# Kernel tuning notes

Hardware: AMD Instinct MI355X
Metric: run time of the kernel (lower is better)

Reference implementation:

```python
import jax, jax.numpy as jnp
import numpy as np

B, T, C, H = 4, 2048, 1024, 16
D = C // H

def setup_inputs() -> dict:
    key = jax.random.key(0)
    k1, k2, k3, k4 = jax.random.split(key, 4)
    s = 1.0 / np.sqrt(C)
    return {
        "x": jax.random.normal(k1, (B, T, C), dtype=jnp.float32),
        "W_qkv": jax.random.normal(k2, (3 * C, C), dtype=jnp.float32) * s,
        "W_out": jax.random.normal(k3, (C, C), dtype=jnp.float32) * s,
        "b_out": jax.random.normal(k4, (C,), dtype=jnp.float32) * s,
    }

def reference(x, W_qkv, W_out, b_out):
    Bx, Tx, Cx = x.shape
    # qkv projection (torch Linear: y = x @ W.T), bias=False
    qkv = x @ W_qkv.T                               # [B,T,3C]
    q, k, v = jnp.split(qkv, 3, axis=-1)
    def heads(t):
        return t.reshape(Bx, Tx, H, D).transpose(0, 2, 1, 3)  # [B,H,T,D]
    q, k, v = heads(q), heads(k), heads(v)
    scale = 1.0 / jnp.sqrt(jnp.asarray(D, dtype=x.dtype))
    scores = jnp.einsum("bhqd,bhkd->bhqk", q, k) * scale      # [B,H,T,T]
    causal = jnp.tril(jnp.ones((Tx, Tx), dtype=bool))
    scores = jnp.where(causal[None, None], scores, -jnp.inf)
    attn = jax.nn.softmax(scores, axis=-1)                    # dropout p=0 (eval)
    out = jnp.einsum("bhqk,bhkd->bhqd", attn, v)              # [B,H,T,D]
    out = out.transpose(0, 2, 1, 3).reshape(Bx, Tx, Cx)       # [B,T,C]
    return out @ W_out.T + b_out
```

## Files before the change

kernel.cpp:

```cpp
#include <hip/hip_runtime.h>


typedef __attribute__((ext_vector_type(8))) __bf16 bf16x8;
typedef __attribute__((ext_vector_type(4))) float f32x4;
typedef __attribute__((ext_vector_type(16))) float f32x16;

__device__ __forceinline__ unsigned short f2bf(float f) {
  union { float f; unsigned u; } v; v.f = f;
  unsigned r = v.u + 0x7fffu + ((v.u >> 16) & 1u);
  return (unsigned short)(r >> 16);
}

__device__ __forceinline__ unsigned cvtpk(float lo, float hi) {
  unsigned r;
  asm("v_cvt_pk_bf16_f32 %0, %1, %2" : "=v"(r) : "v"(lo), "v"(hi));
  return r;
}

__device__ __forceinline__ float fexp2(float x) {
  float r;
  asm("v_exp_f32 %0, %1" : "=v"(r) : "v"(x));
  return r;
}
__device__ __forceinline__ float max3f(float a, float b, float c) {
  return fmaxf(fmaxf(a, b), c);
}

__device__ __forceinline__ void gld16(const void* g, void* l) {
  __builtin_amdgcn_global_load_lds(
      (const __attribute__((address_space(1))) void*)g,
      (__attribute__((address_space(3))) void*)l, 16, 0, 0);
}

__device__ __forceinline__ f32x4 mfma16(bf16x8 a, bf16x8 b, f32x4 c) {
  return __builtin_amdgcn_mfma_f32_16x16x32_bf16(a, b, c, 0, 0, 0);
}
__device__ __forceinline__ f32x16 mfma32(bf16x8 a, bf16x8 b, f32x16 c) {
  return __builtin_amdgcn_mfma_f32_32x32x16_bf16(a, b, c, 0, 0, 0);
}

__global__ __launch_bounds__(256) void cast_f32_bf16(
    const float* __restrict__ src, unsigned short* __restrict__ dst, int n) {
  int i = (blockIdx.x * 256 + threadIdx.x) * 4;
  if (i >= n) return;
  float4 v = *(const float4*)(src + i);
  ushort4 o;
  o.x = f2bf(v.x); o.y = f2bf(v.y); o.z = f2bf(v.z); o.w = f2bf(v.w);
  *(ushort4*)(dst + i) = o;
}

__device__ __forceinline__ bf16x8 ldsw128(const char* mat, int row, int cb) {
  return *(const bf16x8*)(mat + row * 128 + (cb ^ ((row & 7) << 4)));
}

#define PH_SYNC_A() do { __builtin_amdgcn_s_barrier();              \
    asm volatile("s_waitcnt lgkmcnt(0)" ::: "memory");              \
    __builtin_amdgcn_sched_barrier(0); } while (0)
#define PH_SYNC_B() do { __builtin_amdgcn_s_barrier();              \
    __builtin_amdgcn_sched_barrier(0); } while (0)
#define VMC6() asm volatile("s_waitcnt vmcnt(6)" ::: "memory")
#define VMC0() asm volatile("s_waitcnt vmcnt(0)" ::: "memory")

#define QUAD(MH, NH, AF, BF) do {                                   \
    __builtin_amdgcn_s_setprio(1);                                  \
    _Pragma("unroll") for (int mt = 0; mt < 4; ++mt)                \
    _Pragma("unroll") for (int nt = 0; nt < 2; ++nt)                \
    _Pragma("unroll") for (int kk = 0; kk < 2; ++kk)                \
      acc[(MH)*4+mt][(NH)*2+nt] =                                   \
          mfma16(AF[mt][kk], BF[nt][kk], acc[(MH)*4+mt][(NH)*2+nt]);\
    __builtin_amdgcn_s_setprio(0);                                  \
  } while (0)

__device__ __forceinline__ void stage_half(const char* gbase, char* mat,
                                           int kt, int half, int tid) {
#pragma unroll
  for (int q = 0; q < 2; ++q) {
    const int r = half * 128 + q * 64 + (tid >> 3);
    const int cb = (tid & 7) * 16;
    gld16(gbase + (size_t)r * 2048 + kt * 128 + (cb ^ ((r & 7) << 4)),
          mat + r * 128 + cb);
  }
}

__device__ __forceinline__ void rdA(bf16x8 aF[4][2], const char* mat,
                                    int wm, int mh, int lr, int lg) {
#pragma unroll
  for (int mt = 0; mt < 4; ++mt) {
    const int row = mh * 128 + wm * 64 + mt * 16 + lr;
#pragma unroll
    for (int kk = 0; kk < 2; ++kk)
      aF[mt][kk] = ldsw128(mat, row, kk * 64 + lg * 16);
  }
}
__device__ __forceinline__ void rdB(bf16x8 bF[2][2], const char* mat,
                                    int wn, int nh, int lr, int lg) {
#pragma unroll
  for (int nt = 0; nt < 2; ++nt) {
    const int row = wn * 64 + nh * 32 + nt * 16 + lr;
#pragma unroll
    for (int kk = 0; kk < 2; ++kk)
      bF[nt][kk] = ldsw128(mat, row, kk * 64 + lg * 16);
  }
}

template <int MODE>
__global__ __launch_bounds__(512, 2) void gemm8p(
    const unsigned short* __restrict__ A, const unsigned short* __restrict__ Bm,
    unsigned short* __restrict__ qo, unsigned short* __restrict__ ko,
    unsigned short* __restrict__ vo,
    const float* __restrict__ bias, float* __restrict__ fout) {
  __shared__ char lds[131072];
  const int tid = threadIdx.x;
  const int w = tid >> 6, l = tid & 63, lr = l & 15, lg = l >> 4;
  const int wm = w >> 2, wn = w & 3;
  constexpr int GX = (MODE == 0) ? 12 : 4;
  constexpr int NWG = GX * 32;
  const int L = blockIdx.x + blockIdx.y * GX;
  const int logical = (L & 7) * (NWG >> 3) + (L >> 3);
  const int m0 = (logical / GX) * 256, n0 = (logical % GX) * 256;
  const char* Ag = (const char*)A + (size_t)m0 * 2048;
  const char* Bg = (const char*)Bm + (size_t)n0 * 2048;
  char* A0 = lds;           char* B0 = lds + 32768;
  char* A1 = lds + 65536;   char* B1 = lds + 98304;

  f32x4 acc[8][4];
  f32x4 zero = {0.f, 0.f, 0.f, 0.f};
#pragma unroll
  for (int i = 0; i < 8; i++)
#pragma unroll
    for (int jj = 0; jj < 4; jj++) acc[i][jj] = zero;

  stage_half(Ag, A0, 0, 0, tid);
  stage_half(Ag, A0, 0, 1, tid);
  stage_half(Bg, B0, 0, 0, tid);
  stage_half(Bg, B0, 0, 1, tid);
  stage_half(Ag, A1, 1, 0, tid);
  stage_half(Bg, B1, 1, 0, tid);
  stage_half(Bg, B1, 1, 1, tid);
  VMC6();
  __builtin_amdgcn_s_barrier();
  __builtin_amdgcn_sched_barrier(0);

  for (int j = 0; j < 8; ++j) {
    const int t0 = 2 * j, t1 = 2 * j + 1;
    const bool more = (j < 7);
    bf16x8 aF[4][2], b0F[2][2], b1F[2][2];

    rdA(aF, A0, wm, 0, lr, lg);
    rdB(b0F, B0, wn, 0, lr, lg);
    stage_half(Ag, A1, t1, 1, tid);
    PH_SYNC_A();
    QUAD(0, 0, aF, b0F);
    PH_SYNC_B();
    rdB(b1F, B0, wn, 1, lr, lg);
    if (more) stage_half(Ag, A0, t0 + 2, 0, tid);
    PH_SYNC_A();
    QUAD(0, 1, aF, b1F);
    PH_SYNC_B();
    rdA(aF, A0, wm, 1, lr, lg);
    if (more) stage_half(Bg, B0, t0 + 2, 0, tid);
    PH_SYNC_A();
    QUAD(1, 1, aF, b1F);
    PH_SYNC_B();
    if (more) stage_half(Bg, B0, t0 + 2, 1, tid);
    PH_SYNC_A();
    QUAD(1, 0, aF, b0F);
    if (more) VMC6(); else VMC0();
    PH_SYNC_B();
    rdA(aF, A1, wm, 0, lr, lg);
    rdB(b0F, B1, wn, 0, lr, lg);
    if (more) stage_half(Ag, A0, t0 + 2, 1, tid);
    PH_SYNC_A();
    QUAD(0, 0, aF, b0F);
    PH_SYNC_B();
    rdB(b1F, B1, wn, 1, lr, lg);
    if (more) stage_half(Ag, A1, t1 + 2, 0, tid);
    PH_SYNC_A();
    QUAD(0, 1, aF, b1F);
    PH_SYNC_B();
    rdA(aF, A1, wm, 1, lr, lg);
    if (more) stage_half(Bg, B1, t1 + 2, 0, tid);
    PH_SYNC_A();
    QUAD(1, 1, aF, b1F);
    PH_SYNC_B();
    if (more) stage_half(Bg, B1, t1 + 2, 1, tid);
    PH_SYNC_A();
    QUAD(1, 0, aF, b0F);
    if (more) VMC6();
    PH_SYNC_B();
  }

#pragma unroll
  for (int mt8 = 0; mt8 < 8; ++mt8) {
    const int mh = mt8 >> 2, mt = mt8 & 3;
#pragma unroll
    for (int nt4 = 0; nt4 < 4; ++nt4) {
      int n = n0 + wn * 64 + nt4 * 16 + lr;
      int mbase = m0 + mh * 128 + wm * 64 + mt * 16 + lg * 4;
      if (MODE == 0) {
        int ty = n >> 10, cc = n & 1023;
        int h = cc >> 6, dd = cc & 63;
        unsigned short* dst = (ty == 0) ? qo : ((ty == 1) ? ko : vo);
        float sc = (ty == 0) ? 0.18033688011111687f : 1.0f;
#pragma unroll
        for (int i = 0; i < 4; i++) {
          int m = mbase + i;
          int b = m >> 11, tt = m & 2047;
          dst[(((size_t)(b * 16 + h)) * 2048 + tt) * 64 + dd] =
              f2bf(acc[mt8][nt4][i] * sc);
        }
      } else {
        float bv = bias[n];
#pragma unroll
        for (int i = 0; i < 4; i++) {
          int m = mbase + i;
          fout[(size_t)m * 1024 + n] = acc[mt8][nt4][i] + bv;
        }
      }
    }
  }
}

__global__ __launch_bounds__(256) void transpose_v64(
    const unsigned short* __restrict__ v, unsigned short* __restrict__ vt) {
  __shared__ unsigned short tile[64 * 72];
  int bh = blockIdx.y, t0 = blockIdx.x * 64;
  const unsigned short* vp = v + (size_t)bh * 2048 * 64;
  unsigned short* vtp = vt + (size_t)bh * 64 * 2048;
  int tid = threadIdx.x;
#pragma unroll
  for (int it = 0; it < 2; ++it) {
    int s = tid + it * 256;
    int r = s >> 3, c = (s & 7) * 8;
    *(uint4*)(tile + r * 72 + c) = *(const uint4*)(vp + (size_t)(t0 + r) * 64 + c);
  }
  __syncthreads();
#pragma unroll
  for (int it = 0; it < 2; ++it) {
    int s = tid + it * 256;
    int d = s >> 3, c = (s & 7) * 8;
    unsigned short tmp[8];
#pragma unroll
    for (int j = 0; j < 8; j++) tmp[j] = tile[(c + j) * 72 + d];
    *(uint4*)(vtp + (size_t)d * 2048 + t0 + c) = *(uint4*)tmp;
  }
}

__device__ __forceinline__ bf16x8 ldsw(const char* base, int row, int cb) {
  return *(const bf16x8*)(base + row * 128 + (cb ^ ((row & 7) << 4)));
}

__global__ __launch_bounds__(512, 4) void attn_causal(
    const unsigned short* __restrict__ qg, const unsigned short* __restrict__ kg,
    const unsigned short* __restrict__ vtg, unsigned short* __restrict__ og) {
  __shared__ char lds[32768];
  const int tid = threadIdx.x;
  const int w = tid >> 6, l = tid & 63, lo = l & 31, hi = l >> 5;
  const int bh = blockIdx.x;
  const int qc = (0x31204657u >> (blockIdx.y * 4)) & 7;
  const int q0 = qc * 256;
  const int nkv = qc * 4 + 4;
  const int b = bh >> 4, h = bh & 15;
  const char* kpB = (const char*)(kg + (size_t)bh * 131072);
  const char* vpB = (const char*)(vtg + (size_t)bh * 131072);
  const unsigned short* qp = qg + (size_t)bh * 131072;
  const int qrow = q0 + 8 * lo + w;

  bf16x8 qf[4];
#pragma unroll
  for (int c = 0; c < 4; ++c)
    qf[c] = *(const bf16x8*)(qp + (size_t)qrow * 64 + hi * 8 + c * 16);

  f32x16 ov[2];
#pragma unroll
  for (int r = 0; r < 16; ++r) { ov[0][r] = 0.f; ov[1][r] = 0.f; }
  const f32x16 zz = {0.f, 0.f, 0.f, 0.f, 0.f, 0.f, 0.f, 0.f,
                     0.f, 0.f, 0.f, 0.f, 0.f, 0.f, 0.f, 0.f};
  float m = -__builtin_inff(), lsum = 0.f;

  const int srow = tid >> 3;
  const int scb = ((tid & 7) * 16) ^ ((srow & 7) << 4);

  gld16(kpB + (size_t)srow * 128 + scb, lds + tid * 16);
  gld16(vpB + (size_t)srow * 4096 + scb, lds + 8192 + tid * 16);
  __syncthreads();

  for (int kt = 0; kt < nkv; ++kt) {
    const int k0 = kt * 64;
    if (kt + 1 < nkv) {
      char* nb = lds + ((kt + 1) & 1) * 16384;
      gld16(kpB + (size_t)(k0 + 64 + srow) * 128 + scb, nb + tid * 16);
      gld16(vpB + (size_t)srow * 4096 + (size_t)(k0 + 64) * 2 + scb, nb + 8192 + tid * 16);
    }
    const char* Kbuf = lds + (kt & 1) * 16384;
    const char* Vbuf = Kbuf + 8192;

    f32x16 sv[2];
    __builtin_amdgcn_s_setprio(1);
#pragma unroll
    for (int c = 0; c < 4; ++c) {
      bf16x8 kf0 = ldsw(Kbuf, lo, hi * 16 + c * 32);
      bf16x8 kf1 = ldsw(Kbuf, 32 + lo, hi * 16 + c * 32);
      if (c == 0) {
        sv[0] = mfma32(kf0, qf[0], zz);
        sv[1] = mfma32(kf1, qf[0], zz);
      } else {
        sv[0] = mfma32(kf0, qf[c], sv[0]);
        sv[1] = mfma32(kf1, qf[c], sv[1]);
      }
    }
    __builtin_amdgcn_s_setprio(0);

    if (kt >= nkv - 4) {
#pragma unroll
      for (int t = 0; t < 2; ++t)
#pragma unroll
        for (int r = 0; r < 16; ++r) {
          int kgl = k0 + t * 32 + (r & 3) + 8 * (r >> 2) + 4 * hi;
          if (kgl > qrow) sv[t][r] = -__builtin_inff();
        }
    }

    float t0m = max3f(sv[0][0], sv[0][1], sv[0][2]);
    float t1m = max3f(sv[0][3], sv[0][4], sv[0][5]);
    float t2m = max3f(sv[0][6], sv[0][7], sv[0][8]);
    float t3m = max3f(sv[0][9], sv[0][10], sv[0][11]);
    float t4m = max3f(sv[0][12], sv[0][13], sv[0][14]);
    float t5m = max3f(sv[0][15], sv[1][0], sv[1][1]);
    float t6m = max3f(sv[1][2], sv[1][3], sv[1][4]);
    float t7m = max3f(sv[1][5], sv[1][6], sv[1][7]);
    float t8m = max3f(sv[1][8], sv[1][9], sv[1][10]);
    float t9m = max3f(sv[1][11], sv[1][12], sv[1][13]);
    float tam = fmaxf(sv[1][14], sv[1][15]);
    float u0 = max3f(t0m, t1m, t2m);
    float u1 = max3f(t3m, t4m, t5m);
    float u2 = max3f(t6m, t7m, t8m);
    float u3 = fmaxf(t9m, tam);
    float tm = fmaxf(max3f(u0, u1, u2), u3);
    tm = fmaxf(tm, __shfl_xor(tm, 32, 64));

    if (!__all(tm <= m + 8.f)) {
      float nm = fmaxf(fmaxf(m, tm), -1e30f);
      float f = fexp2(m - nm);
      m = nm;
      lsum *= f;
#pragma unroll
      for (int r = 0; r < 16; ++r) { ov[0][r] *= f; ov[1][r] *= f; }
    }

    float ps0 = 0.f, ps1 = 0.f, ps2 = 0.f, ps3 = 0.f;
#pragma unroll
    for (int t = 0; t < 2; ++t)
#pragma unroll
      for (int r = 0; r < 16; r += 4) {
        float p0 = fexp2(sv[t][r + 0] - m);
        float p1 = fexp2(sv[t][r + 1] - m);
        float p2 = fexp2(sv[t][r + 2] - m);
        float p3 = fexp2(sv[t][r + 3] - m);
        sv[t][r + 0] = p0; sv[t][r + 1] = p1;
        sv[t][r + 2] = p2; sv[t][r + 3] = p3;
        ps0 += p0; ps1 += p1; ps2 += p2; ps3 += p3;
      }
    lsum += (ps0 + ps1) + (ps2 + ps3);

    __builtin_amdgcn_s_setprio(1);
#pragma unroll
    for (int c = 0; c < 4; ++c) {
      const int t = c >> 1, rb = (c & 1) * 8;
      unsigned wA = cvtpk(sv[t][rb + 0], sv[t][rb + 1]);
      unsigned wB = cvtpk(sv[t][rb + 2], sv[t][rb + 3]);
      unsigned wC = cvtpk(sv[t][rb + 4], sv[t][rb + 5]);
      unsigned wD = cvtpk(sv[t][rb + 6], sv[t][rb + 7]);
      asm volatile("v_permlane32_swap_b32 %0, %1" : "+v"(wA), "+v"(wC));
      asm volatile("v_permlane32_swap_b32 %0, %1" : "+v"(wB), "+v"(wD));
      union { uint4 u; bf16x8 h; } pc;
      pc.u.x = wA; pc.u.y = wB; pc.u.z = wC; pc.u.w = wD;
      bf16x8 vf0 = ldsw(Vbuf, lo, hi * 16 + c * 32);
      bf16x8 vf1 = ldsw(Vbuf, 32 + lo, hi * 16 + c * 32);
      ov[0] = mfma32(vf0, pc.h, ov[0]);
      ov[1] = mfma32(vf1, pc.h, ov[1]);
    }
    __builtin_amdgcn_s_setprio(0);
    __syncthreads();
  }

  float lt = lsum + __shfl_xor(lsum, 32, 64);
  float inv = 1.0f / lt;
  char* outl = lds + w * 4096;
#pragma unroll
  for (int t2 = 0; t2 < 2; ++t2)
#pragma unroll
    for (int rp = 0; rp < 8; ++rp) {
      const int r = rp * 2;
      const int d0 = (r & 3) + 8 * (r >> 2) + 4 * hi + 32 * t2;
      unsigned pw = cvtpk(ov[t2][r] * inv, ov[t2][r + 1] * inv);
      *(unsigned*)(outl + lo * 128 + ((d0 * 2) ^ ((lo & 7) << 4))) = pw;
    }
  __syncthreads();
  {
    const int qi = l >> 1, cbb = (l & 1) * 64;
    const int t = q0 + 8 * qi + w;
    unsigned short* gp = og + ((size_t)(b * 2048 + t)) * 1024 + h * 64 + (cbb >> 1);
#pragma unroll
    for (int i = 0; i < 4; ++i) {
      uint4 vdat = *(const uint4*)(outl + qi * 128 + ((cbb + i * 16) ^ ((qi & 7) << 4)));
      *(uint4*)(gp + i * 8) = vdat;
    }
  }
}

extern "C" void kernel_launch(void* const* d_in, const int* in_sizes, int n_in,
                              void* d_out, int out_size, void* d_ws, size_t ws_size,
                              hipStream_t stream) {
  const float* x = (const float*)d_in[0];
  const float* Wqkv = (const float*)d_in[1];
  const float* Wout = (const float*)d_in[2];
  const float* bout = (const float*)d_in[3];
  float* out = (float*)d_out;
  char* ws = (char*)d_ws;

  unsigned short* xb = (unsigned short*)(ws);
  unsigned short* wqb = (unsigned short*)(ws + 16777216);
  unsigned short* wob = (unsigned short*)(ws + 23068672);
  unsigned short* qb = (unsigned short*)(ws + 25165824);
  unsigned short* kb = (unsigned short*)(ws + 41943040);
  unsigned short* vb = (unsigned short*)(ws + 58720256);
  unsigned short* vtb = xb;
  unsigned short* ogb = vb;

  cast_f32_bf16<<<8192, 256, 0, stream>>>(x, xb, 8388608);
  cast_f32_bf16<<<3072, 256, 0, stream>>>(Wqkv, wqb, 3145728);
  cast_f32_bf16<<<1024, 256, 0, stream>>>(Wout, wob, 1048576);

  gemm8p<0><<<dim3(12, 32), 512, 0, stream>>>(xb, wqb, qb, kb, vb, nullptr, nullptr);
  transpose_v64<<<dim3(32, 64), 256, 0, stream>>>(vb, vtb);
  attn_causal<<<dim3(64, 8), 512, 0, stream>>>(qb, kb, vtb, ogb);
  gemm8p<1><<<dim3(4, 32), 512, 0, stream>>>(ogb, wob, nullptr, nullptr, nullptr, bout, out);
}
```

Before: 169.0 us.

## Fuse V transpose into QKV GEMM epilogue with LDS-staged coalesced stores

The QKV GEMM epilogue now stages its bf16 output tile in LDS with an XOR swizzle. It then writes Q/K rows as coalesced 16-byte chunks, and writes V already transposed into the [B,H,D,T] layout that attention reads. This drops the separate transpose kernel and its extra global round trip, and replaces the scattered 2-byte global stores. The workgroup-to-tile mapping also changes so each XCD group covers contiguous M tiles. The cost is an extra barrier and LDS traffic in the epilogue, and the workspace buffers are remapped.

```diff
diff --git a/kernel.cpp b/kernel.cpp
--- a/kernel.cpp
+++ b/kernel.cpp
@@ -51,6 +51,9 @@
 
 __device__ __forceinline__ bf16x8 ldsw128(const char* mat, int row, int cb) {
   return *(const bf16x8*)(mat + row * 128 + (cb ^ ((row & 7) << 4)));
+}
+__device__ __forceinline__ int swz512(int r) {
+  return ((r & 7) << 4) ^ (((r >> 3) & 3) << 7);
 }
 
 #define PH_SYNC_A() do { __builtin_amdgcn_s_barrier();              \
@@ -114,10 +117,10 @@
   const int w = tid >> 6, l = tid & 63, lr = l & 15, lg = l >> 4;
   const int wm = w >> 2, wn = w & 3;
   constexpr int GX = (MODE == 0) ? 12 : 4;
-  constexpr int NWG = GX * 32;
   const int L = blockIdx.x + blockIdx.y * GX;
-  const int logical = (L & 7) * (NWG >> 3) + (L >> 3);
-  const int m0 = (logical / GX) * 256, n0 = (logical % GX) * 256;
+  const int x = L & 7, i8 = L >> 3;
+  const int m0 = (x * 4 + (i8 & 3)) * 256;
+  const int n0 = (i8 >> 2) * 256;
   const char* Ag = (const char*)A + (size_t)m0 * 2048;
   const char* Bg = (const char*)Bm + (size_t)n0 * 2048;
   char* A0 = lds;           char* B0 = lds + 32768;
@@ -190,59 +193,85 @@
     PH_SYNC_B();
   }
 
-#pragma unroll
-  for (int mt8 = 0; mt8 < 8; ++mt8) {
-    const int mh = mt8 >> 2, mt = mt8 & 3;
-#pragma unroll
-    for (int nt4 = 0; nt4 < 4; ++nt4) {
-      int n = n0 + wn * 64 + nt4 * 16 + lr;
-      int mbase = m0 + mh * 128 + wm * 64 + mt * 16 + lg * 4;
-      if (MODE == 0) {
-        int ty = n >> 10, cc = n & 1023;
-        int h = cc >> 6, dd = cc & 63;
-        unsigned short* dst = (ty == 0) ? qo : ((ty == 1) ? ko : vo);
-        float sc = (ty == 0) ? 0.18033688011111687f : 1.0f;
-#pragma unroll
-        for (int i = 0; i < 4; i++) {
-          int m = mbase + i;
-          int b = m >> 11, tt = m & 2047;
-          dst[(((size_t)(b * 16 + h)) * 2048 + tt) * 64 + dd] =
+  if (MODE == 1) {
+#pragma unroll
+    for (int mt8 = 0; mt8 < 8; ++mt8) {
+      const int mh = mt8 >> 2, mt = mt8 & 3;
+#pragma unroll
+      for (int nt4 = 0; nt4 < 4; ++nt4) {
+        int n = n0 + wn * 64 + nt4 * 16 + lr;
+        int mbase = m0 + mh * 128 + wm * 64 + mt * 16 + lg * 4;
+        float bv = bias[n];
+#pragma unroll
+        for (int i = 0; i < 4; i++)
+          fout[(size_t)(mbase + i) * 1024 + n] = acc[mt8][nt4][i] + bv;
+      }
+    }
+    return;
+  }
+
+  const int ty = n0 >> 10;
+  const int hbase = (n0 & 1023) >> 6;
+  const int bb = m0 >> 11;
+  const int tloc = m0 & 2047;
+  const float sc = (ty == 0) ? 0.18033688011111687f : 1.0f;
+
+  if (ty < 2) {
+#pragma unroll
+    for (int mt8 = 0; mt8 < 8; ++mt8) {
+      const int mh = mt8 >> 2, mt = mt8 & 3;
+#pragma unroll
+      for (int nt4 = 0; nt4 < 4; ++nt4) {
+        const int col = wn * 64 + nt4 * 16 + lr;
+#pragma unroll
+        for (int i = 0; i < 4; ++i) {
+          const int row = mh * 128 + wm * 64 + mt * 16 + lg * 4 + i;
+          *(unsigned short*)(lds + row * 512 + ((col * 2) ^ swz512(row))) =
               f2bf(acc[mt8][nt4][i] * sc);
         }
-      } else {
-        float bv = bias[n];
-#pragma unroll
-        for (int i = 0; i < 4; i++) {
-          int m = mbase + i;
-          fout[(size_t)m * 1024 + n] = acc[mt8][nt4][i] + bv;
-        }
-      }
-    }
-  }
-}
-
-__global__ __launch_bounds__(256) void transpose_v64(
-    const unsigned short* __restrict__ v, unsigned short* __restrict__ vt) {
-  __shared__ unsigned short tile[64 * 72];
-  int bh = blockIdx.y, t0 = blockIdx.x * 64;
-  const unsigned short* vp = v + (size_t)bh * 2048 * 64;
-  unsigned short* vtp = vt + (size_t)bh * 64 * 2048;
-  int tid = threadIdx.x;
-#pragma unroll
-  for (int it = 0; it < 2; ++it) {
-    int s = tid + it * 256;
-    int r = s >> 3, c = (s & 7) * 8;
-    *(uint4*)(tile + r * 72 + c) = *(const uint4*)(vp + (size_t)(t0 + r) * 64 + c);
-  }
-  __syncthreads();
-#pragma unroll
-  for (int it = 0; it < 2; ++it) {
-    int s = tid + it * 256;
-    int d = s >> 3, c = (s & 7) * 8;
-    unsigned short tmp[8];
-#pragma unroll
-    for (int j = 0; j < 8; j++) tmp[j] = tile[(c + j) * 72 + d];
-    *(uint4*)(vtp + (size_t)d * 2048 + t0 + c) = *(uint4*)tmp;
+      }
+    }
+    __builtin_amdgcn_s_barrier();
+    unsigned short* dst = (ty == 0) ? qo : ko;
+    const int hi = tid >> 7, r = tid & 127;
+    unsigned short* gp =
+        dst + (((size_t)(bb * 16 + hbase + hi)) * 2048 + tloc + 2 * r) * 64;
+#pragma unroll
+    for (int rr = 0; rr < 2; ++rr) {
+      const int row = 2 * r + rr;
+#pragma unroll
+      for (int jc = 0; jc < 8; ++jc) {
+        uint4 vd = *(const uint4*)(lds + row * 512 +
+                                   ((hi * 128 + jc * 16) ^ swz512(row)));
+        *(uint4*)(gp + rr * 64 + jc * 8) = vd;
+      }
+    }
+  } else {
+#pragma unroll
+    for (int mt8 = 0; mt8 < 8; ++mt8) {
+      const int mh = mt8 >> 2, mt = mt8 & 3;
+      const int mcb = (mh * 128 + wm * 64 + mt * 16 + lg * 4) * 2;
+#pragma unroll
+      for (int nt4 = 0; nt4 < 4; ++nt4) {
+        const int row = wn * 64 + nt4 * 16 + lr;
+        uint2 pk;
+        pk.x = cvtpk(acc[mt8][nt4][0], acc[mt8][nt4][1]);
+        pk.y = cvtpk(acc[mt8][nt4][2], acc[mt8][nt4][3]);
+        *(uint2*)(lds + row * 512 + (mcb ^ swz512(row))) = pk;
+      }
+    }
+    __builtin_amdgcn_s_barrier();
+    const int hi = tid >> 7, r = tid & 127;
+    const int dd = r >> 1, mh2 = r & 1;
+    const int nrow = hi * 64 + dd;
+    unsigned short* gp = vo +
+        (((size_t)(bb * 16 + hbase + hi)) * 64 + dd) * 2048 + tloc + mh2 * 128;
+#pragma unroll
+    for (int jc = 0; jc < 16; ++jc) {
+      uint4 vd = *(const uint4*)(lds + nrow * 512 +
+                                 ((mh2 * 256 + jc * 16) ^ swz512(nrow)));
+      *(uint4*)(gp + jc * 8) = vd;
+    }
   }
 }
 
@@ -424,16 +453,14 @@
   unsigned short* wob = (unsigned short*)(ws + 23068672);
   unsigned short* qb = (unsigned short*)(ws + 25165824);
   unsigned short* kb = (unsigned short*)(ws + 41943040);
-  unsigned short* vb = (unsigned short*)(ws + 58720256);
-  unsigned short* vtb = xb;
-  unsigned short* ogb = vb;
+  unsigned short* vtb = (unsigned short*)(ws + 58720256);
+  unsigned short* ogb = xb;
 
   cast_f32_bf16<<<8192, 256, 0, stream>>>(x, xb, 8388608);
   cast_f32_bf16<<<3072, 256, 0, stream>>>(Wqkv, wqb, 3145728);
   cast_f32_bf16<<<1024, 256, 0, stream>>>(Wout, wob, 1048576);
 
-  gemm8p<0><<<dim3(12, 32), 512, 0, stream>>>(xb, wqb, qb, kb, vb, nullptr, nullptr);
-  transpose_v64<<<dim3(32, 64), 256, 0, stream>>>(vb, vtb);
+  gemm8p<0><<<dim3(12, 32), 512, 0, stream>>>(xb, wqb, qb, kb, vtb, nullptr, nullptr);
   attn_causal<<<dim3(64, 8), 512, 0, stream>>>(qb, kb, vtb, ogb);
   gemm8p<1><<<dim3(4, 32), 512, 0, stream>>>(ogb, wob, nullptr, nullptr, nullptr, bout, out);
 }
```

Result: no change. 172.0 us (+1.8%).
